# Kernel tuning notes

Hardware: AMD Instinct MI355X
Metric: run time of the kernel (lower is better)

## Reference

```python
import jax, jax.numpy as jnp
import numpy as np
from jax import lax

RATE, STRIDE, KSIZE, FUSE_K, SCALE = 2, 1, 3, 3, 10.0


def img2col(img, k, s):
    # torch F.unfold with padding=1, reshaped to [B, L, C, k, k] (L row-major over patch grid)
    B, C, H, W = img.shape
    p = jnp.pad(img, ((0, 0), (0, 0), (1, 1), (1, 1)))
    nH = (H + 2 - k) // s + 1
    nW = (W + 2 - k) // s + 1
    slabs = [p[:, :, ki:ki + s * (nH - 1) + 1:s, kj:kj + s * (nW - 1) + 1:s]
             for ki in range(k) for kj in range(k)]
    pats = jnp.stack(slabs, axis=2).reshape(B, C, k, k, nH, nW)
    return pats.transpose(0, 4, 5, 1, 2, 3).reshape(B, nH * nW, C, k, k)


def diag_prop(M, fk):
    # conv2d of the [L, L] score matrix with an identity fuse kernel == sum over diagonal shifts
    r = fk // 2
    B, L, _ = M.shape
    Mp = jnp.pad(M, ((0, 0), (r, r), (r, r)))
    out = jnp.zeros_like(M)
    for d in range(-r, r + 1):
        out = out + Mp[:, r + d:r + d + L, r + d:r + d + L]
    return out


def _fwd(foreground, background, mask):
    pad = KSIZE // 2
    # raw-resolution background patches used for reconstruction: [B, L, C, 2*rate, 2*rate]
    cols = img2col(background, 2 * RATE, RATE * STRIDE)
    # nearest-neighbor downsample by rate (torch F.interpolate scale_factor=1/rate, mode='nearest')
    fg = foreground[:, :, ::RATE, ::RATE]
    bg = background[:, :, ::RATE, ::RATE]
    m = mask[:, :, ::RATE, ::RATE]
    mask_cols = img2col(m, KSIZE, STRIDE)            # [B, L, 1, 3, 3]
    masked = jnp.sum(mask_cols, axis=(2, 3, 4)) == 0.0  # [B, L]
    kern = img2col(bg, KSIZE, STRIDE)                # [B, L, C, 3, 3]
    denom = jnp.sqrt(jnp.sum(kern * kern, axis=(2, 3, 4), keepdims=True))
    kern = kern / jnp.maximum(denom, 1e-3)

    def conv_one(img, k_):  # img [C,h,w], k_ [L,C,3,3] -> [L,h,w]
        return lax.conv_general_dilated(img[None], k_, (1, 1), [(pad, pad), (pad, pad)],
                                        dimension_numbers=('NCHW', 'OIHW', 'NCHW'))[0]

    scores = jax.vmap(conv_one)(fg, kern)            # [B, L, h, w]
    B, L, h, w = scores.shape
    # attention propagation: identity-kernel conv over [h*w, h*w], both orientations
    M = diag_prop(scores.reshape(B, L, h * w), FUSE_K)
    M = M.reshape(B, h, w, h, w).transpose(0, 2, 1, 4, 3).reshape(B, h * w, h * w)
    M = diag_prop(M, FUSE_K)
    scores = M.reshape(B, h, w, h, w).transpose(0, 2, 1, 4, 3).reshape(B, L, h, w)
    scores = jnp.where(masked[:, :, None, None], -1000.0, scores)
    soft = jax.nn.softmax(SCALE * scores, axis=1)

    kt = 2 * RATE
    tpad = kt - 1 - pad  # conv_transpose2d(stride=rate, padding=pad) as dilated conv

    def deconv_one(s_, t_):  # s_ [L,h,w], t_ [L,C,kt,kt] -> [C,H,W]
        W2 = jnp.flip(jnp.transpose(t_, (1, 0, 2, 3)), (2, 3))  # [C,L,kt,kt]
        return lax.conv_general_dilated(s_[None], W2, (1, 1), [(tpad, tpad), (tpad, tpad)],
                                        lhs_dilation=(RATE, RATE),
                                        dimension_numbers=('NCHW', 'OIHW', 'NCHW'))[0]

    return jax.vmap(deconv_one)(soft, cols)          # [B, C, H, W]


def setup_inputs() -> dict:
    key = jax.random.key(0)
    kf, kb, km = jax.random.split(key, 3)
    B, C, H, W = 2, 64, 128, 128
    foreground = jax.random.normal(kf, (B, C, H, W), jnp.float32)
    background = jax.random.normal(kb, (B, C, H, W), jnp.float32)
    mask = (jax.random.uniform(km, (B, 1, H, W)) > 0.5).astype(jnp.float32)
    return {"foreground": foreground, "background": background, "mask": mask}


def reference(foreground, background, mask):
    return _fwd(foreground, background, mask)
```

## Files before the change

kernel.cpp:

```cpp
#include <hip/hip_runtime.h>
#include <hip/hip_bf16.h>

#define B_ 2
#define C_ 64
#define H_ 128
#define W_ 128
#define HS 64
#define WS 64
#define L_ 4096
#define S_ 4096
#define K1_ 576
#define NCOL 1024
#define SCALE_ 10.0f

typedef __attribute__((ext_vector_type(8))) short bf16x8;
typedef __attribute__((ext_vector_type(8))) _Float16 f16x8;
typedef __attribute__((ext_vector_type(4))) float f32x4;

__device__ __forceinline__ void async_copy16(const void* gsrc, void* ldst) {
    __builtin_amdgcn_global_load_lds(
        (__attribute__((address_space(1))) const void*)gsrc,
        (__attribute__((address_space(3))) void*)ldst, 16, 0, 0);
}

__device__ __forceinline__ int TT(int x) { return ((x & 63) << 6) | (x >> 6); }

__device__ __forceinline__ float diag3Y(const float* __restrict__ Y, int l, int s) {
    int tl = TT(l), ts = TT(s);
    float acc = 0.f;
#pragma unroll
    for (int d2 = -1; d2 <= 1; ++d2) {
        int p = tl + d2, q = ts + d2;
        if ((unsigned)p < 4096u && (unsigned)q < 4096u)
            acc += Y[((size_t)TT(p) << 12) + TT(q)];
    }
    return acc;
}

__global__ void k_sumsq(const float* __restrict__ bg, float* __restrict__ ssq) {
    int idx = blockIdx.x * 256 + threadIdx.x;
    if (idx >= B_ * HS * WS) return;
    int pix = idx & 4095, b = idx >> 12;
    int i = pix >> 6, j = pix & 63;
    float ss = 0.f;
    for (int c = 0; c < C_; ++c) {
        float v = bg[((b * C_ + c) * H_ + 2 * i) * W_ + 2 * j];
        ss += v * v;
    }
    ssq[idx] = ss;
}

__global__ void k_patch_stats(const float* __restrict__ mask, const float* __restrict__ ssq,
                              float* __restrict__ denom_inv, float* __restrict__ maskedf) {
    int idx = blockIdx.x * 256 + threadIdx.x;
    if (idx >= B_ * L_) return;
    int b = idx >> 12, l = idx & 4095, lh = l >> 6, lw = l & 63;
    float msum = 0.f, ss = 0.f;
    for (int di = -1; di <= 1; ++di)
        for (int dj = -1; dj <= 1; ++dj) {
            int i = lh + di, j = lw + dj;
            if (i >= 0 && i < HS && j >= 0 && j < WS) {
                msum += mask[(b * H_ + 2 * i) * W_ + 2 * j];
                ss += ssq[(b << 12) + (i << 6) + j];
            }
        }
    maskedf[idx] = (msum == 0.0f) ? 1.0f : 0.0f;
    denom_inv[idx] = 1.0f / fmaxf(sqrtf(ss), 0.001f);
}

__global__ void k_prep(const float* __restrict__ bgb, const float* __restrict__ fgb,
                       _Float16* __restrict__ bcol, _Float16* __restrict__ fcol,
                       __hip_bfloat16* __restrict__ colsT) {
    int idx = blockIdx.x * 256 + threadIdx.x;
    if (idx < 2 * L_ * K1_) {
        int which = idx >= L_ * K1_;
        int id = which ? idx - L_ * K1_ : idx;
        const float* src = which ? fgb : bgb;
        _Float16* dst = which ? fcol : bcol;
        int k = id % K1_;
        int l = id / K1_;
        int c = k / 9, r = k - 9 * c;
        int r3 = r / 3;
        int di = r3 - 1, dj = r - 3 * r3 - 1;
        int i = (l >> 6) + di, j = (l & 63) + dj;
        float v = 0.f;
        if (i >= 0 && i < HS && j >= 0 && j < WS) v = src[(c * H_ + 2 * i) * W_ + 2 * j];
        dst[id] = (_Float16)v;
    } else {
        int id = idx - 2 * L_ * K1_;
        int l = id & 4095, n = id >> 12;
        int kj = n & 3, ki = (n >> 2) & 3, c = n >> 4;
        int y = 2 * (l >> 6) + ki - 1, x = 2 * (l & 63) + kj - 1;
        float v = 0.f;
        if (y >= 0 && y < H_ && x >= 0 && x < W_) v = bgb[(c * H_ + y) * W_ + x];
        colsT[id] = __float2bfloat16(v);
    }
}

__global__ __launch_bounds__(256) void k_gemm1_mfma(const _Float16* __restrict__ A,
                                                    const _Float16* __restrict__ Bm,
                                                    const float* __restrict__ dinv,
                                                    float* __restrict__ scores,
                                                    float* __restrict__ Y) {
    __shared__ __align__(16) char shraw[128 * 129 * 4];
    int t = threadIdx.x, lane = t & 63, w = t >> 6;
    int wm = w & 1, wn = w >> 1;
    int M0 = blockIdx.y * 128, N0 = blockIdx.x * 128;
    f32x4 acc[4][4] = {};

    auto stage = [&](int k0, int offh) {
        _Float16* Asb = (_Float16*)shraw + offh;
        _Float16* Bsb = Asb + 8192;
#pragma unroll
        for (int rp = 0; rp < 4; ++rp) {
            int chunk = rp * 256 + t;
            int row = chunk >> 3;
            int kc = (chunk & 7) ^ (row & 7);
            async_copy16(A + (size_t)(M0 + row) * K1_ + k0 + kc * 8, &Asb[chunk * 8]);
        }
#pragma unroll
        for (int rp = 0; rp < 4; ++rp) {
            int chunk = rp * 256 + t;
            int row = chunk >> 3;
            int kc = (chunk & 7) ^ (row & 7);
            async_copy16(Bm + (size_t)(N0 + row) * K1_ + k0 + kc * 8, &Bsb[chunk * 8]);
        }
    };

    stage(0, 0);
    int buf = 0;
    for (int k0 = 0; k0 < K1_; k0 += 64) {
        if (k0 + 64 < K1_) {
            stage(k0 + 64, (buf ^ 1) * 16384);
            asm volatile("s_waitcnt vmcnt(8)" ::: "memory");
        } else {
            asm volatile("s_waitcnt vmcnt(0)" ::: "memory");
        }
        __builtin_amdgcn_s_barrier();
        _Float16* As = (_Float16*)shraw + buf * 16384;
        _Float16* Bs = As + 8192;
        int qc = lane >> 4, mr = lane & 15;
#pragma unroll
        for (int kk = 0; kk < 2; ++kk) {
            int c = kk * 4 + qc;
            f16x8 af[4], bfr[4];
#pragma unroll
            for (int i = 0; i < 4; ++i) {
                int ra = wm * 64 + i * 16 + mr;
                int rb = wn * 64 + i * 16 + mr;
                af[i] = *(const f16x8*)&As[ra * 64 + (c ^ (ra & 7)) * 8];
                bfr[i] = *(const f16x8*)&Bs[rb * 64 + (c ^ (rb & 7)) * 8];
            }
#pragma unroll
            for (int mt = 0; mt < 4; ++mt)
#pragma unroll
                for (int nt = 0; nt < 4; ++nt)
                    acc[mt][nt] = __builtin_amdgcn_mfma_f32_16x16x32_f16(af[mt], bfr[nt], acc[mt][nt], 0, 0, 0);
        }
        __builtin_amdgcn_s_barrier();
        buf ^= 1;
    }
    int col = lane & 15, rq = (lane >> 4) * 4;
#pragma unroll
    for (int mt = 0; mt < 4; ++mt)
#pragma unroll
        for (int r = 0; r < 4; ++r) {
            int ml = wm * 64 + mt * 16 + rq + r;
            bool rstrip = (ml <= 1) || (ml >= 126);
            float dv = dinv[M0 + ml];
#pragma unroll
            for (int nt = 0; nt < 4; ++nt) {
                int nl = wn * 64 + nt * 16 + col;
                bool cstrip = (nl <= 1) || (nl >= 126);
                if (rstrip || cstrip)
                    scores[((size_t)(M0 + ml) << 12) + N0 + nl] = acc[mt][nt][r] * dv;
            }
        }
    float* sm = (float*)shraw;
#pragma unroll
    for (int mt = 0; mt < 4; ++mt)
#pragma unroll
        for (int r = 0; r < 4; ++r) {
            int ml = wm * 64 + mt * 16 + rq + r;
            float dv = dinv[M0 + ml];
#pragma unroll
            for (int nt = 0; nt < 4; ++nt) {
                int nl = wn * 64 + nt * 16 + col;
                sm[ml * 129 + nl] = acc[mt][nt][r] * dv;
            }
        }
    __syncthreads();
    for (int e = t; e < 126 * 128; e += 256) {
        int rr = 1 + (e >> 7);
        int cc = e & 127;
        if (cc < 1 || cc > 126) continue;
        float y = sm[(rr - 1) * 129 + cc - 1] + sm[rr * 129 + cc] + sm[(rr + 1) * 129 + cc + 1];
        Y[((size_t)(M0 + rr) << 12) + N0 + cc] = y;
    }
}

__global__ void k_pass1_edge(const float* __restrict__ scores, float* __restrict__ Y) {
    int idx = blockIdx.x * 256 + threadIdx.x;
    int a, c;
    if (idx < 262144) {
        int ri = idx >> 12;
        a = (ri >> 1) * 128 + ((ri & 1) ? 127 : 0);
        c = idx & 4095;
    } else {
        int j = idx - 262144;
        int ci = j >> 12;
        c = (ci >> 1) * 128 + ((ci & 1) ? 127 : 0);
        a = j & 4095;
    }
    float acc = 0.f;
#pragma unroll
    for (int d = -1; d <= 1; ++d) {
        int aa = a + d, cc = c + d;
        if ((unsigned)aa < 4096u && (unsigned)cc < 4096u)
            acc += scores[((size_t)aa << 12) + cc];
    }
    Y[((size_t)a << 12) + c] = acc;
}

__global__ __launch_bounds__(256) void k_soft3(const float* __restrict__ Y,
                                               const float* __restrict__ maskedf,
                                               __hip_bfloat16* __restrict__ softT,
                                               float* __restrict__ pml, float* __restrict__ pz) {
    __shared__ float tile[64][65];
    __shared__ float red[16][64];
    __shared__ float mloc[64];
    int t = threadIdx.x;
    int sx4 = t & 15, lg = t >> 4;
    int bid = blockIdx.x;
    int swz = (bid & 7) * 512 + (bid >> 3);
    int dg = swz >> 6, pos = swz & 63;
    int by = pos, bx = (pos + dg) & 63;
    int s0 = bx * 64, l0 = by * 64;
    bool interior = (bx >= 1) && (bx <= 62) && (by >= 1) && (by <= 62);
    float p0 = -3.0e38f, p1 = -3.0e38f, p2 = -3.0e38f, p3 = -3.0e38f;
    if (interior) {
        float4 v[12];
        float mk[4];
#pragma unroll
        for (int j = 0; j < 4; ++j) {
            int lloc = lg + 16 * j;
#pragma unroll
            for (int d2 = 0; d2 < 3; ++d2) {
                const float* p = Y + ((size_t)(64 * (by + d2 - 1) + lloc) << 12) + 64 * (bx + d2 - 1) + 4 * sx4;
                v[j * 3 + d2] = *(const float4*)p;
            }
        }
#pragma unroll
        for (int j = 0; j < 4; ++j) mk[j] = maskedf[l0 + lg + 16 * j];
#pragma unroll
        for (int j = 0; j < 4; ++j) {
            int lloc = lg + 16 * j;
            float a0 = v[j * 3].x + v[j * 3 + 1].x + v[j * 3 + 2].x;
            float a1 = v[j * 3].y + v[j * 3 + 1].y + v[j * 3 + 2].y;
            float a2 = v[j * 3].z + v[j * 3 + 1].z + v[j * 3 + 2].z;
            float a3 = v[j * 3].w + v[j * 3 + 1].w + v[j * 3 + 2].w;
            if (mk[j] != 0.f) { a0 = -1000.f; a1 = -1000.f; a2 = -1000.f; a3 = -1000.f; }
            tile[lloc][4 * sx4 + 0] = a0;
            tile[lloc][4 * sx4 + 1] = a1;
            tile[lloc][4 * sx4 + 2] = a2;
            tile[lloc][4 * sx4 + 3] = a3;
            p0 = fmaxf(p0, a0); p1 = fmaxf(p1, a1); p2 = fmaxf(p2, a2); p3 = fmaxf(p3, a3);
        }
    } else {
#pragma unroll
        for (int j = 0; j < 4; ++j) {
            int lloc = lg + 16 * j;
            int l = l0 + lloc;
            bool mk = (maskedf[l] != 0.f);
            float a0 = mk ? -1000.f : diag3Y(Y, l, s0 + 4 * sx4 + 0);
            float a1 = mk ? -1000.f : diag3Y(Y, l, s0 + 4 * sx4 + 1);
            float a2 = mk ? -1000.f : diag3Y(Y, l, s0 + 4 * sx4 + 2);
            float a3 = mk ? -1000.f : diag3Y(Y, l, s0 + 4 * sx4 + 3);
            tile[lloc][4 * sx4 + 0] = a0;
            tile[lloc][4 * sx4 + 1] = a1;
            tile[lloc][4 * sx4 + 2] = a2;
            tile[lloc][4 * sx4 + 3] = a3;
            p0 = fmaxf(p0, a0); p1 = fmaxf(p1, a1); p2 = fmaxf(p2, a2); p3 = fmaxf(p3, a3);
        }
    }
    red[lg][4 * sx4 + 0] = p0;
    red[lg][4 * sx4 + 1] = p1;
    red[lg][4 * sx4 + 2] = p2;
    red[lg][4 * sx4 + 3] = p3;
    __syncthreads();
    if (t < 64) {
        float m = -3.0e38f;
#pragma unroll
        for (int g = 0; g < 16; ++g) m = fmaxf(m, red[g][t]);
        mloc[t] = m;
        pml[(size_t)(s0 + t) * 64 + by] = m;
    }
    __syncthreads();
    float m0 = mloc[4 * sx4 + 0], m1 = mloc[4 * sx4 + 1], m2 = mloc[4 * sx4 + 2], m3 = mloc[4 * sx4 + 3];
    float z0 = 0.f, z1 = 0.f, z2 = 0.f, z3 = 0.f;
#pragma unroll
    for (int j = 0; j < 4; ++j) {
        int lloc = lg + 16 * j;
        float e0 = __expf(SCALE_ * (tile[lloc][4 * sx4 + 0] - m0));
        float e1 = __expf(SCALE_ * (tile[lloc][4 * sx4 + 1] - m1));
        float e2 = __expf(SCALE_ * (tile[lloc][4 * sx4 + 2] - m2));
        float e3 = __expf(SCALE_ * (tile[lloc][4 * sx4 + 3] - m3));
        tile[lloc][4 * sx4 + 0] = e0;
        tile[lloc][4 * sx4 + 1] = e1;
        tile[lloc][4 * sx4 + 2] = e2;
        tile[lloc][4 * sx4 + 3] = e3;
        z0 += e0; z1 += e1; z2 += e2; z3 += e3;
    }
    red[lg][4 * sx4 + 0] = z0;
    red[lg][4 * sx4 + 1] = z1;
    red[lg][4 * sx4 + 2] = z2;
    red[lg][4 * sx4 + 3] = z3;
    __syncthreads();
    if (t < 64) {
        float zz = 0.f;
#pragma unroll
        for (int g = 0; g < 16; ++g) zz += red[g][t];
        pz[(size_t)(s0 + t) * 64 + by] = zz;
    }
#pragma unroll
    for (int pp = 0; pp < 2; ++pp) {
        int chunk = pp * 256 + t;
        int sloc = chunk >> 3, lb = (chunk & 7) * 8;
        bf16x8 o;
#pragma unroll
        for (int k = 0; k < 8; ++k) {
            __hip_bfloat16 r = __float2bfloat16(tile[lb + k][sloc]);
            o[k] = *reinterpret_cast<short*>(&r);
        }
        *(bf16x8*)(softT + ((size_t)(s0 + sloc) << 12) + l0 + lb) = o;
    }
}

__global__ __launch_bounds__(256) void k_zr(const float* __restrict__ pml,
                                            const float* __restrict__ pz,
                                            __hip_bfloat16* __restrict__ softT) {
    __shared__ float facs[64];
    int t = threadIdx.x;
    int s = blockIdx.x;
    if (t < 64) {
        float pmv = pml[(size_t)s * 64 + t];
        float m = pmv;
#pragma unroll
        for (int off = 1; off < 64; off <<= 1) m = fmaxf(m, __shfl_xor(m, off));
        float fc = __expf(SCALE_ * (pmv - m));
        float g = pz[(size_t)s * 64 + t] * fc;
#pragma unroll
        for (int off = 1; off < 64; off <<= 1) g += __shfl_xor(g, off);
        facs[t] = fc * (1.0f / g);
    }
    __syncthreads();
    size_t rowbase = (size_t)s << 12;
#pragma unroll
    for (int p = 0; p < 2; ++p) {
        int chunk = t + p * 256;
        float f = facs[chunk >> 3];
        bf16x8 v = *(const bf16x8*)(softT + rowbase + chunk * 8);
        bf16x8 o;
#pragma unroll
        for (int k = 0; k < 8; ++k) {
            unsigned short us = (unsigned short)v[k];
            float x = __uint_as_float((unsigned)us << 16) * f;
            __hip_bfloat16 r = __float2bfloat16(x);
            o[k] = *reinterpret_cast<short*>(&r);
        }
        *(bf16x8*)(softT + rowbase + chunk * 8) = o;
    }
}

__global__ __launch_bounds__(256) void k_gemm2_mfma(const __hip_bfloat16* __restrict__ softT,
                                                    const __hip_bfloat16* __restrict__ colsT,
                                                    float* __restrict__ patchP) {
    __shared__ __hip_bfloat16 AsB[2][12288];
    int t = threadIdx.x, lane = t & 63, w = t >> 6;
    int wm = w & 1, wn = w >> 1;
    int flat = blockIdx.x + (blockIdx.y << 4) + (blockIdx.z << 9);
    int xp = (flat >> 3) & 15;
    int yp = (flat & 7) | (((flat >> 7) & 3) << 3);
    int zp = flat >> 9;
    int M0 = yp * 128, N0 = xp * 64;
    int kbase = zp * 2048;
    f32x4 acc[4][2] = {};

    auto stage = [&](int k0, int bsel) {
        __hip_bfloat16* Asb = AsB[bsel];
        __hip_bfloat16* Bsb = Asb + 8192;
#pragma unroll
        for (int rp = 0; rp < 4; ++rp) {
            int chunk = rp * 256 + t;
            int row = chunk >> 3;
            int kc = (chunk & 7) ^ (row & 7);
            async_copy16(softT + ((size_t)(M0 + row) << 12) + k0 + kc * 8, &Asb[chunk * 8]);
        }
#pragma unroll
        for (int rp = 0; rp < 2; ++rp) {
            int chunk = rp * 256 + t;
            int row = chunk >> 3;
            int kc = (chunk & 7) ^ (row & 7);
            async_copy16(colsT + ((size_t)(N0 + row) << 12) + k0 + kc * 8, &Bsb[chunk * 8]);
        }
    };

    stage(kbase, 0);
    int buf = 0;
    for (int k0 = kbase; k0 < kbase + 2048; k0 += 64) {
        if (k0 + 64 < kbase + 2048) {
            stage(k0 + 64, buf ^ 1);
            asm volatile("s_waitcnt vmcnt(6)" ::: "memory");
        } else {
            asm volatile("s_waitcnt vmcnt(0)" ::: "memory");
        }
        __builtin_amdgcn_s_barrier();
        __hip_bfloat16* As = AsB[buf];
        __hip_bfloat16* Bs = As + 8192;
        int qc = lane >> 4, mr = lane & 15;
#pragma unroll
        for (int kk = 0; kk < 2; ++kk) {
            int c = kk * 4 + qc;
            bf16x8 af[4], bfr[2];
#pragma unroll
            for (int i = 0; i < 4; ++i) {
                int rowa = wm * 64 + i * 16 + mr;
                af[i] = *(const bf16x8*)&As[rowa * 64 + (c ^ (rowa & 7)) * 8];
            }
#pragma unroll
            for (int j = 0; j < 2; ++j) {
                int rowb = wn * 32 + j * 16 + mr;
                bfr[j] = *(const bf16x8*)&Bs[rowb * 64 + (c ^ (rowb & 7)) * 8];
            }
#pragma unroll
            for (int mt = 0; mt < 4; ++mt)
#pragma unroll
                for (int nt = 0; nt < 2; ++nt)
                    acc[mt][nt] = __builtin_amdgcn_mfma_f32_16x16x32_bf16(af[mt], bfr[nt], acc[mt][nt], 0, 0, 0);
        }
        __builtin_amdgcn_s_barrier();
        buf ^= 1;
    }
    float* P = patchP + ((size_t)zp << 22);
    int col = lane & 15, rq = (lane >> 4) * 4;
#pragma unroll
    for (int mt = 0; mt < 4; ++mt)
#pragma unroll
        for (int r = 0; r < 4; ++r) {
            int m = M0 + wm * 64 + mt * 16 + rq + r;
#pragma unroll
            for (int nt = 0; nt < 2; ++nt) {
                int n = N0 + wn * 32 + nt * 16 + col;
                P[(size_t)m * 1024 + n] = acc[mt][nt][r];
            }
        }
}

__global__ void k_col2im(const float* __restrict__ patchP, float* __restrict__ outb) {
    int idx = blockIdx.x * 256 + threadIdx.x;
    if (idx >= C_ * H_ * W_) return;
    int x = idx & 127, y = (idx >> 7) & 127, c = idx >> 14;
    const float* P0 = patchP;
    const float* P1 = patchP + (1u << 22);
    float acc = 0.f;
    int ki0 = (y + 1) & 1, kj0 = (x + 1) & 1;
#pragma unroll
    for (int ki = ki0; ki < 4; ki += 2) {
        int i = (y + 1 - ki) >> 1;
        if (i < 0 || i >= HS) continue;
#pragma unroll
        for (int kj = kj0; kj < 4; kj += 2) {
            int j = (x + 1 - kj) >> 1;
            if (j < 0 || j >= WS) continue;
            size_t off = ((size_t)(i * 64 + j) << 10) + c * 16 + ki * 4 + kj;
            acc += P0[off] + P1[off];
        }
    }
    outb[idx] = acc;
}

extern "C" void kernel_launch(void* const* d_in, const int* in_sizes, int n_in,
                              void* d_out, int out_size, void* d_ws, size_t ws_size,
                              hipStream_t stream) {
    (void)in_sizes; (void)n_in; (void)out_size; (void)ws_size;
    const float* fg = (const float*)d_in[0];
    const float* bg = (const float*)d_in[1];
    const float* mask = (const float*)d_in[2];
    float* out = (float*)d_out;

    float* ws = (float*)d_ws;
    float* scores = ws;
    float* patchP = ws;
    float* Y = ws + 16777216;
    _Float16* bgcol = (_Float16*)(ws + 33554432);
    _Float16* fgcol = (_Float16*)(ws + 34734080);
    __hip_bfloat16* softT = (__hip_bfloat16*)(ws + 38273024);
    __hip_bfloat16* colsT = (__hip_bfloat16*)(ws + 46661632);
    float* pml = ws + 48758784;
    float* pz = ws + 49020928;
    float* denom_inv = ws + 49283072;
    float* maskedf = ws + 49291264;
    float* ssq = ws + 49299456;

    k_sumsq<<<(B_ * HS * WS) / 256, 256, 0, stream>>>(bg, ssq);
    k_patch_stats<<<(B_ * L_) / 256, 256, 0, stream>>>(mask, ssq, denom_inv, maskedf);

    for (int b = 0; b < B_; ++b) {
        const float* bgb = bg + (size_t)b * C_ * H_ * W_;
        const float* fgb = fg + (size_t)b * C_ * H_ * W_;

        k_prep<<<(2 * L_ * K1_ + NCOL * L_) / 256, 256, 0, stream>>>(bgb, fgb, bgcol, fgcol, colsT);

        dim3 g1(32, 32);
        k_gemm1_mfma<<<g1, 256, 0, stream>>>(bgcol, fgcol, denom_inv + b * L_, scores, Y);
        k_pass1_edge<<<2048, 256, 0, stream>>>(scores, Y);

        k_soft3<<<4096, 256, 0, stream>>>(Y, maskedf + b * L_, softT, pml, pz);
        k_zr<<<4096, 256, 0, stream>>>(pml, pz, softT);

        dim3 g5(16, 32, 2);
        k_gemm2_mfma<<<g5, 256, 0, stream>>>(softT, colsT, patchP);
        k_col2im<<<(C_ * H_ * W_) / 256, 256, 0, stream>>>(patchP, out + (size_t)b * C_ * H_ * W_);
    }
}
```

Before: 443.0 us.

## Enlarge gemm2 tile to 128x128, drop double buffering, remap block swizzle

Changes the second GEMM (softmax × patch columns) to use 128x128 output tiles with a 4x4 MFMA accumulator per wave, halving the grid in N. The double-buffered async LDS prefetch is replaced by a single buffer with __syncthreads around each K-step, and the block-to-tile swizzle is redone. The larger tile raises operand reuse and arithmetic intensity but loses load/compute overlap and doubles accumulator registers. Whether the sync-based single buffer correctly waits for the async LDS loads is also less explicit than before.

```diff
diff --git a/kernel.cpp b/kernel.cpp
--- a/kernel.cpp
+++ b/kernel.cpp
@@ -375,71 +375,52 @@
 __global__ __launch_bounds__(256) void k_gemm2_mfma(const __hip_bfloat16* __restrict__ softT,
                                                     const __hip_bfloat16* __restrict__ colsT,
                                                     float* __restrict__ patchP) {
-    __shared__ __hip_bfloat16 AsB[2][12288];
+    __shared__ __hip_bfloat16 As[128 * 64], Bs[128 * 64];
     int t = threadIdx.x, lane = t & 63, w = t >> 6;
     int wm = w & 1, wn = w >> 1;
-    int flat = blockIdx.x + (blockIdx.y << 4) + (blockIdx.z << 9);
-    int xp = (flat >> 3) & 15;
-    int yp = (flat & 7) | (((flat >> 7) & 3) << 3);
-    int zp = flat >> 9;
-    int M0 = yp * 128, N0 = xp * 64;
+    int flat = blockIdx.x + (blockIdx.y << 3) + (blockIdx.z << 8);
+    int swz = (flat & 7) * 64 + (flat >> 3);
+    int zp = swz >> 8;
+    int rem = swz & 255;
+    int yp = rem >> 3, xp = rem & 7;
+    int M0 = yp * 128, N0 = xp * 128;
     int kbase = zp * 2048;
-    f32x4 acc[4][2] = {};
-
-    auto stage = [&](int k0, int bsel) {
-        __hip_bfloat16* Asb = AsB[bsel];
-        __hip_bfloat16* Bsb = Asb + 8192;
+    f32x4 acc[4][4] = {};
+    for (int k0 = kbase; k0 < kbase + 2048; k0 += 64) {
 #pragma unroll
         for (int rp = 0; rp < 4; ++rp) {
             int chunk = rp * 256 + t;
             int row = chunk >> 3;
             int kc = (chunk & 7) ^ (row & 7);
-            async_copy16(softT + ((size_t)(M0 + row) << 12) + k0 + kc * 8, &Asb[chunk * 8]);
-        }
-#pragma unroll
-        for (int rp = 0; rp < 2; ++rp) {
+            async_copy16(softT + ((size_t)(M0 + row) << 12) + k0 + kc * 8, &As[chunk * 8]);
+        }
+#pragma unroll
+        for (int rp = 0; rp < 4; ++rp) {
             int chunk = rp * 256 + t;
             int row = chunk >> 3;
             int kc = (chunk & 7) ^ (row & 7);
-            async_copy16(colsT + ((size_t)(N0 + row) << 12) + k0 + kc * 8, &Bsb[chunk * 8]);
-        }
-    };
-
-    stage(kbase, 0);
-    int buf = 0;
-    for (int k0 = kbase; k0 < kbase + 2048; k0 += 64) {
-        if (k0 + 64 < kbase + 2048) {
-            stage(k0 + 64, buf ^ 1);
-            asm volatile("s_waitcnt vmcnt(6)" ::: "memory");
-        } else {
-            asm volatile("s_waitcnt vmcnt(0)" ::: "memory");
-        }
-        __builtin_amdgcn_s_barrier();
-        __hip_bfloat16* As = AsB[buf];
-        __hip_bfloat16* Bs = As + 8192;
+            async_copy16(colsT + ((size_t)(N0 + row) << 12) + k0 + kc * 8, &Bs[chunk * 8]);
+        }
+        __syncthreads();
         int qc = lane >> 4, mr = lane & 15;
 #pragma unroll
         for (int kk = 0; kk < 2; ++kk) {
             int c = kk * 4 + qc;
-            bf16x8 af[4], bfr[2];
+            bf16x8 af[4], bfr[4];
 #pragma unroll
             for (int i = 0; i < 4; ++i) {
                 int rowa = wm * 64 + i * 16 + mr;
                 af[i] = *(const bf16x8*)&As[rowa * 64 + (c ^ (rowa & 7)) * 8];
-            }
-#pragma unroll
-            for (int j = 0; j < 2; ++j) {
-                int rowb = wn * 32 + j * 16 + mr;
-                bfr[j] = *(const bf16x8*)&Bs[rowb * 64 + (c ^ (rowb & 7)) * 8];
+                int rowb = wn * 64 + i * 16 + mr;
+                bfr[i] = *(const bf16x8*)&Bs[rowb * 64 + (c ^ (rowb & 7)) * 8];
             }
 #pragma unroll
             for (int mt = 0; mt < 4; ++mt)
 #pragma unroll
-                for (int nt = 0; nt < 2; ++nt)
+                for (int nt = 0; nt < 4; ++nt)
                     acc[mt][nt] = __builtin_amdgcn_mfma_f32_16x16x32_bf16(af[mt], bfr[nt], acc[mt][nt], 0, 0, 0);
         }
-        __builtin_amdgcn_s_barrier();
-        buf ^= 1;
+        __syncthreads();
     }
     float* P = patchP + ((size_t)zp << 22);
     int col = lane & 15, rq = (lane >> 4) * 4;
@@ -449,8 +430,8 @@
         for (int r = 0; r < 4; ++r) {
             int m = M0 + wm * 64 + mt * 16 + rq + r;
 #pragma unroll
-            for (int nt = 0; nt < 2; ++nt) {
-                int n = N0 + wn * 32 + nt * 16 + col;
+            for (int nt = 0; nt < 4; ++nt) {
+                int n = N0 + wn * 64 + nt * 16 + col;
                 P[(size_t)m * 1024 + n] = acc[mt][nt][r];
             }
         }
@@ -518,7 +499,7 @@
         k_soft3<<<4096, 256, 0, stream>>>(Y, maskedf + b * L_, softT, pml, pz);
         k_zr<<<4096, 256, 0, stream>>>(pml, pz, softT);
 
-        dim3 g5(16, 32, 2);
+        dim3 g5(8, 32, 2);
         k_gemm2_mfma<<<g5, 256, 0, stream>>>(softT, colsT, patchP);
         k_col2im<<<(C_ * H_ * W_) / 256, 256, 0, stream>>>(patchP, out + (size_t)b * C_ * H_ * W_);
     }
```

After: 435.5 us. About the same (-1.7%).
